# Kernel tuning notes

Hardware: AMD Instinct MI355X
Metric: run time of the kernel (lower is better)

## Reference

```python
import jax, jax.numpy as jnp
import numpy as np

B, N, D_IN, H, D_OUT = 64, 512, 1024, 1024, 1024
EPS = 1e-5          # torch BatchNorm1d default eps
NEG_SLOPE = 0.01    # torch leaky_relu default


def setup_inputs() -> dict:
    key = jax.random.key(0)
    ks = jax.random.split(key, 12)
    s_in = 1.0 / np.sqrt(D_IN)
    s_h = 1.0 / np.sqrt(H)
    return {
        "x": jax.random.normal(ks[0], (B, N, D_IN), dtype=jnp.float32),
        # weights stored as [in, out] so y = x @ W + b
        "W1": jax.random.uniform(ks[1], (D_IN, H), jnp.float32, -s_in, s_in),
        "b1": jax.random.uniform(ks[2], (H,), jnp.float32, -s_in, s_in),
        "gamma": jnp.ones((N,), jnp.float32),
        "beta": jnp.zeros((N,), jnp.float32),
        "W2": jax.random.uniform(ks[3], (D_IN, H), jnp.float32, -s_in, s_in),
        "b2": jax.random.uniform(ks[4], (H,), jnp.float32, -s_in, s_in),
        "W3": jax.random.uniform(ks[5], (H, D_OUT), jnp.float32, -s_h, s_h),
        "b3": jax.random.uniform(ks[6], (D_OUT,), jnp.float32, -s_h, s_h),
        "W4": jax.random.uniform(ks[7], (D_IN, D_OUT), jnp.float32, -s_in, s_in),
        "b4": jax.random.uniform(ks[8], (D_OUT,), jnp.float32, -s_in, s_in),
    }


def reference(x, W1, b1, gamma, beta, W2, b2, W3, b3, W4, b4):
    h = W1.shape[1]
    # theta_x = leaky_relu(bn(l1(x)))
    t = x @ W1 + b1                                   # [B, N, H]
    # BatchNorm1d(num_input): channel dim is N; train-mode batch stats over (B, H)
    mean = jnp.mean(t, axis=(0, 2), keepdims=True)
    var = jnp.var(t, axis=(0, 2), keepdims=True)      # biased variance (torch norm path)
    t = gamma[None, :, None] * (t - mean) * jax.lax.rsqrt(var + EPS) + beta[None, :, None]
    t = jnp.where(t >= 0, t, NEG_SLOPE * t)
    # sigma = theta @ M @ theta^T with M = (I - 1/h)/h  ==  mean-center rows then scale by 1/h
    tM = (t - jnp.mean(t, axis=-1, keepdims=True)) / h  # [B, N, H]
    sigma = jnp.einsum("bnh,bmh->bnm", tM, t)           # [B, N, N]
    att = sigma / jnp.sqrt(jnp.float32(h))              # normal_factor = sqrt(hidden)
    # GLOBAL softmax over the full flattened N*N matrix per batch element
    bsz, n = x.shape[0], x.shape[1]
    att = jax.nn.softmax(att.reshape(bsz, -1), axis=1).reshape(bsz, n, n)
    g = x @ W2 + b2                                     # [B, N, H]
    p = jnp.einsum("bnm,bmh->bnh", att, g) @ W3 + b3    # [B, N, D_OUT]
    phi = x @ W4 + b4                                   # [B, N, D_OUT]
    return phi + p
```

## Files before the change

kernel.cpp:

```cpp
#include <hip/hip_runtime.h>
#include <hip/hip_bf16.h>

typedef _Float16 f16x8 __attribute__((ext_vector_type(8)));
typedef _Float16 f16x4 __attribute__((ext_vector_type(4)));
typedef float    f32x4 __attribute__((ext_vector_type(4)));

#define EPS_ 1e-5f

__device__ __forceinline__ void gload_lds16(const _Float16* g, _Float16* l) {
    __builtin_amdgcn_global_load_lds(
        (const __attribute__((address_space(1))) void*)g,
        (__attribute__((address_space(3))) void*)l, 16, 0, 0);
}


__global__ void k_cvt_f16(const float* __restrict__ in, _Float16* __restrict__ out, int n4) {
    int i = blockIdx.x * blockDim.x + threadIdx.x;
    int stride = gridDim.x * blockDim.x;
    const float4* in4 = (const float4*)in;
    for (; i < n4; i += stride) {
        float4 v = in4[i];
        f16x4 o;
        o[0] = (_Float16)v.x; o[1] = (_Float16)v.y;
        o[2] = (_Float16)v.z; o[3] = (_Float16)v.w;
        *(f16x4*)(out + (size_t)i * 4) = o;
    }
}

__global__ void k_transpose_w(const float* __restrict__ in, _Float16* __restrict__ out) {
    __shared__ float tile[32][33];
    int bx = blockIdx.x * 32;
    int by = blockIdx.y * 32;
    int tx = threadIdx.x, ty = threadIdx.y;
    #pragma unroll
    for (int r = 0; r < 32; r += 8)
        tile[ty + r][tx] = in[(size_t)(by + ty + r) * 1024 + bx + tx];
    __syncthreads();
    #pragma unroll
    for (int r = 0; r < 32; r += 8)
        out[(size_t)(bx + ty + r) * 1024 + by + tx] = (_Float16)tile[tx][ty + r];
}

__global__ void k_b23(const float* __restrict__ b2, const float* __restrict__ W3,
                      float* __restrict__ b23) {
    const int oo = threadIdx.x & 63, hc = threadIdx.x >> 6;
    const int o = blockIdx.x * 64 + oo;
    float s = 0.f;
    for (int h = hc * 256; h < hc * 256 + 256; ++h) s += b2[h] * W3[(size_t)h * 1024 + o];
    __shared__ float red[4][64];
    red[hc][oo] = s;
    __syncthreads();
    if (threadIdx.x < 64) {
        int o2 = blockIdx.x * 64 + threadIdx.x;
        b23[o2] = red[0][threadIdx.x] + red[1][threadIdx.x] + red[2][threadIdx.x] + red[3][threadIdx.x];
    }
}


__global__ void k_bnstats(const _Float16* __restrict__ t, const float* __restrict__ gamma,
                          const float* __restrict__ beta, float* __restrict__ scale,
                          float* __restrict__ shift) {
    const int n = blockIdx.x, tid = threadIdx.x;
    float s = 0.f, s2 = 0.f;
    const _Float16* base = t + (size_t)n * 1024 + tid * 4;
    for (int b = 0; b < 64; ++b) {
        f16x4 v = *(const f16x4*)(base + (size_t)b * 512 * 1024);
        float x0 = (float)v[0], x1 = (float)v[1], x2 = (float)v[2], x3 = (float)v[3];
        s  += x0 + x1 + x2 + x3;
        s2 += x0 * x0 + x1 * x1 + x2 * x2 + x3 * x3;
    }
    #pragma unroll
    for (int o = 32; o > 0; o >>= 1) { s += __shfl_down(s, o); s2 += __shfl_down(s2, o); }
    __shared__ float rs_[4], rs2_[4];
    int lane = tid & 63, w = tid >> 6;
    if (lane == 0) { rs_[w] = s; rs2_[w] = s2; }
    __syncthreads();
    if (tid == 0) {
        float S  = rs_[0] + rs_[1] + rs_[2] + rs_[3];
        float S2 = rs2_[0] + rs2_[1] + rs2_[2] + rs2_[3];
        float mean = S * (1.f / 65536.f);
        float var  = S2 * (1.f / 65536.f) - mean * mean;
        float r = rsqrtf(var + EPS_);
        float sc = gamma[n] * r;
        scale[n] = sc;
        shift[n] = beta[n] - mean * sc;
    }
}

__global__ void k_bnorm(const _Float16* __restrict__ t, const float* __restrict__ scale,
                        const float* __restrict__ shift, _Float16* __restrict__ theta,
                        float* __restrict__ mu) {
    const int row = blockIdx.x, tid = threadIdx.x;
    const int n = row & 511;
    const float sc = scale[n], sh = shift[n];
    f16x4 v = *(const f16x4*)(t + (size_t)row * 1024 + tid * 4);
    float a0 = fmaf((float)v[0], sc, sh); a0 = a0 >= 0.f ? a0 : 0.01f * a0;
    float a1 = fmaf((float)v[1], sc, sh); a1 = a1 >= 0.f ? a1 : 0.01f * a1;
    float a2 = fmaf((float)v[2], sc, sh); a2 = a2 >= 0.f ? a2 : 0.01f * a2;
    float a3 = fmaf((float)v[3], sc, sh); a3 = a3 >= 0.f ? a3 : 0.01f * a3;
    float s = a0 + a1 + a2 + a3;
    #pragma unroll
    for (int o = 32; o > 0; o >>= 1) s += __shfl_down(s, o);
    __shared__ float red[4];
    int lane = tid & 63, w = tid >> 6;
    if (lane == 0) red[w] = s;
    __syncthreads();
    const float mean = (red[0] + red[1] + red[2] + red[3]) * (1.f / 1024.f);
    f16x4 th;
    th[0] = (_Float16)a0; th[1] = (_Float16)a1; th[2] = (_Float16)a2; th[3] = (_Float16)a3;
    *(f16x4*)(theta + (size_t)row * 1024 + tid * 4) = th;
    if (tid == 0) mu[row] = mean;
}

__global__ void k_ssum(const float* __restrict__ part, float* __restrict__ rsum,
                       float* __restrict__ ssum) {
    const int b = blockIdx.x, j = threadIdx.x;
    const int idx = b * 512 + j;
    float s = part[idx] + part[32768 + idx] + part[65536 + idx] + part[98304 + idx];
    rsum[idx] = s;
    #pragma unroll
    for (int o = 32; o > 0; o >>= 1) s += __shfl_down(s, o);
    __shared__ float red[8];
    if ((j & 63) == 0) red[j >> 6] = s;
    __syncthreads();
    if (j == 0) {
        float tt = 0.f;
        #pragma unroll
        for (int k = 0; k < 8; k++) tt += red[k];
        ssum[b] = tt;
    }
}


template <int MODE>
__global__ __launch_bounds__(256) void k_gemm(
    const _Float16* __restrict__ A0, const _Float16* __restrict__ B0,
    const float* __restrict__ auxA, float* __restrict__ auxW,
    void* __restrict__ outp) {

    constexpr int BK = 32;
    __shared__ _Float16 Al[4096];
    __shared__ _Float16 Bl[4096];

    const int tid = threadIdx.x, lane = tid & 63, w = tid >> 6;
    const int wm = w >> 1, wn = w & 1;
    const int bm = blockIdx.x, bn = blockIdx.y, bz = blockIdx.z;

    const int srow = tid >> 2;
    const int skofs = ((tid & 3) ^ ((tid >> 3) & 3)) * 8;
    _Float16* lA0 = &Al[(w * 64) * 8];
    _Float16* lA1 = &Al[(256 + w * 64) * 8];
    _Float16* lB0 = &Bl[(w * 64) * 8];
    _Float16* lB1 = &Bl[(256 + w * 64) * 8];

    const int lr = lane & 15, kg = lane >> 4;
    const int kswz = kg ^ ((lr >> 1) & 3);

    f32x4 acc[4][4] = {};

    const size_t aO = ((size_t)bz * 512 + bm * 128) * 1024;
    const size_t bO = ((size_t)bz * 512 + bn * 128) * 1024;
    for (int k0 = 0; k0 < 1024; k0 += BK) {
        gload_lds16(A0 + aO + (size_t)srow * 1024 + k0 + skofs, lA0);
        gload_lds16(A0 + aO + (size_t)(srow + 64) * 1024 + k0 + skofs, lA1);
        gload_lds16(B0 + bO + (size_t)srow * 1024 + k0 + skofs, lB0);
        gload_lds16(B0 + bO + (size_t)(srow + 64) * 1024 + k0 + skofs, lB1);
        __syncthreads();
        f16x8 af[4], bf[4];
        #pragma unroll
        for (int m = 0; m < 4; m++)
            af[m] = *(const f16x8*)&Al[((wm * 64 + m * 16 + lr) * 4 + kswz) * 8];
        #pragma unroll
        for (int n = 0; n < 4; n++)
            bf[n] = *(const f16x8*)&Bl[((wn * 64 + n * 16 + lr) * 4 + kswz) * 8];
        #pragma unroll
        for (int m = 0; m < 4; m++)
            #pragma unroll
            for (int n = 0; n < 4; n++)
                acc[m][n] = __builtin_amdgcn_mfma_f32_16x16x32_f16(af[m], bf[n], acc[m][n], 0, 0, 0);
        __syncthreads();
    }

    if constexpr (MODE == 1) {
        __shared__ float rbuf[2][128];
        _Float16* o = (_Float16*)outp + (size_t)bz * 262144;
        #pragma unroll
        for (int m = 0; m < 4; m++) {
            const int r0 = wm * 64 + m * 16 + kg * 4;
            float rs[4] = {0.f, 0.f, 0.f, 0.f};
            #pragma unroll
            for (int n = 0; n < 4; n++) {
                const int gc = bn * 128 + wn * 64 + n * 16 + lr;
                const float mj = auxA[bz * 512 + gc];
                #pragma unroll
                for (int i = 0; i < 4; i++) {
                    const float mi = auxA[bz * 512 + bm * 128 + r0 + i];
                    const float e = __expf(acc[m][n][i] * (1.f / 32768.f) - mi * mj * (1.f / 32.f));
                    o[(size_t)(bm * 128 + r0 + i) * 512 + gc] = (_Float16)e;
                    rs[i] += e;
                }
            }
            #pragma unroll
            for (int i = 0; i < 4; i++) {
                float v = rs[i];
                v += __shfl_xor(v, 1); v += __shfl_xor(v, 2);
                v += __shfl_xor(v, 4); v += __shfl_xor(v, 8);
                if (lr == 0) rbuf[wn][r0 + i] = v;
            }
        }
        __syncthreads();
        if (tid < 128)
            auxW[(size_t)bn * 32768 + bz * 512 + bm * 128 + tid] = rbuf[0][tid] + rbuf[1][tid];
    } else {
        _Float16* o = (_Float16*)outp;
        #pragma unroll
        for (int m = 0; m < 4; m++) {
            #pragma unroll
            for (int n = 0; n < 4; n++) {
                const int r0 = wm * 64 + m * 16 + kg * 4;
                const int gc = bn * 128 + wn * 64 + n * 16 + lr;
                #pragma unroll
                for (int i = 0; i < 4; i++)
                    o[(size_t)(bm * 128 + r0 + i) * 1024 + gc] = (_Float16)acc[m][n][i];
            }
        }
    }
}


template <int MODE>
__global__ __launch_bounds__(512) void k_gemm8(
    const _Float16* __restrict__ A0, const _Float16* __restrict__ B0,
    const _Float16* __restrict__ A1, const _Float16* __restrict__ B1,
    const float* __restrict__ biasf, const float* __restrict__ biasg,
    const float* __restrict__ auxA, const float* __restrict__ auxB,
    const float* __restrict__ sumptr, void* __restrict__ outp) {

    __shared__ _Float16 LA[32768];
    __shared__ _Float16 LB[32768];

    const int tid = threadIdx.x, lane = tid & 63, wid = tid >> 6;
    const int wm = wid >> 2, wn = wid & 3;
    const int lr = lane & 15, kq = lane >> 4;

    const int swz = (blockIdx.x & 7) * 64 + (blockIdx.x >> 3);
    int bm, bn, bz = 0;
    if constexpr (MODE == 3) { bz = swz >> 3; bm = (swz >> 2) & 1; bn = swz & 3; }
    else { bm = swz >> 2; bn = swz & 3; }

    constexpr int NITER = (MODE == 3) ? 12 : 8;
    float oscale = 1.f;
    if constexpr (MODE == 3) oscale = 1.f / sumptr[bz];

    const int i0 = tid >> 3;
    const int kgs = (tid & 7) ^ (i0 & 7);

    auto STAGE = [&](int g, int isA, int h) {
        const _Float16* P; int ld; size_t off; int kk;
        if constexpr (MODE == 3) {
            if (g < 8) {
                kk = g * 64;
                if (isA) { P = A0; ld = 512;  off = (size_t)bz * 262144 + (size_t)bm * 256 * 512; }
                else     { P = B0; ld = 512;  off = (size_t)bz * 524288 + (size_t)bn * 256 * 512; }
            } else {
                kk = (g - 8) * 64;
                if (isA) { P = A1; ld = 1024; off = ((size_t)bz * 512 + bm * 256) * 1024; }
                else     { P = B1; ld = 1024; off = (size_t)bn * 256 * 1024; }
            }
        } else {
            kk = g * 64;
            if (isA) { P = A0; ld = 1024; off = (size_t)bm * 256 * 1024; }
            else     { P = B0; ld = 1024; off = (size_t)bn * 256 * 1024; }
        }
        const int l0 = isA ? (h * 64 + i0)
                           : ((i0 >> 5) * 64 + h * 32 + (i0 & 31));
        const int l1 = isA ? (128 + h * 64 + i0)
                           : (((i0 >> 5) + 2) * 64 + h * 32 + (i0 & 31));
        _Float16* dst = (isA ? LA : LB) + ((g & 1) * 2 + h) * 8192 + wid * 512;
        gload_lds16(P + off + (size_t)l0 * ld + kk + kgs * 8, dst);
        gload_lds16(P + off + (size_t)l1 * ld + kk + kgs * 8, dst + 4096);
    };

    f32x4 acc[8][4] = {};

    STAGE(0, 1, 0); STAGE(0, 0, 0); STAGE(0, 0, 1); STAGE(0, 1, 1);
    STAGE(1, 0, 0); STAGE(1, 0, 1); STAGE(1, 1, 0);
    asm volatile("s_waitcnt vmcnt(6)" ::: "memory");
    __builtin_amdgcn_s_barrier();

    for (int i = 0; i < NITER; ++i) {
        if constexpr (MODE == 3) {
            if (i == 4) {
                #pragma unroll
                for (int m = 0; m < 8; m++)
                    #pragma unroll
                    for (int n = 0; n < 4; n++)
                        #pragma unroll
                        for (int v = 0; v < 4; v++) acc[m][n][v] *= oscale;
            }
        }
        const bool more = (i + 1 < NITER);
        #pragma unroll
        for (int kt = 0; kt < 2; ++kt) {
            f16x8 bf[4][2];
            #pragma unroll
            for (int sub = 0; sub < 4; ++sub) {
                const int ph = kt * 4 + sub;
                if (sub == 0) {
                    #pragma unroll
                    for (int n = 0; n < 4; n++) {
                        const _Float16* Bs = LB + (kt * 2 + (n >> 1)) * 8192;
                        #pragma unroll
                        for (int s = 0; s < 2; s++)
                            bf[n][s] = *(const f16x8*)&Bs[(wn * 32 + (n & 1) * 16 + lr) * 64
                                                           + ((((s << 2) | kq) ^ (lr & 7)) << 3)];
                    }
                }
                const _Float16* As = LA + (kt * 2 + (sub >> 1)) * 8192;
                f16x8 af[2][2];
                #pragma unroll
                for (int j = 0; j < 2; j++) {
                    const int m = sub * 2 + j;
                    #pragma unroll
                    for (int s = 0; s < 2; s++)
                        af[j][s] = *(const f16x8*)&As[(wm * 64 + (m & 3) * 16 + lr) * 64
                                                       + ((((s << 2) | kq) ^ (lr & 7)) << 3)];
                }
                {
                    constexpr int gof[8] = {1, 2, 2, 2, 2, 3, 3, 3};
                    constexpr int isa[8] = {1, 0, 0, 1, 1, 0, 0, 1};
                    constexpr int hh [8] = {1, 0, 1, 0, 1, 0, 1, 0};
                    if (ph == 0 || more) STAGE(2 * i + gof[ph], isa[ph], hh[ph]);
                }
                __builtin_amdgcn_s_barrier();
                asm volatile("s_waitcnt lgkmcnt(0)" ::: "memory");
                __builtin_amdgcn_sched_barrier(0);
                __builtin_amdgcn_s_setprio(1);
                #pragma unroll
                for (int j = 0; j < 2; j++)
                    #pragma unroll
                    for (int n = 0; n < 4; n++)
                        #pragma unroll
                        for (int s = 0; s < 2; s++)
                            acc[sub * 2 + j][n] = __builtin_amdgcn_mfma_f32_16x16x32_f16(
                                af[j][s], bf[n][s], acc[sub * 2 + j][n], 0, 0, 0);
                __builtin_amdgcn_s_setprio(0);
                if (ph == 1) { if (more) asm volatile("s_waitcnt vmcnt(10)" ::: "memory");
                               else      asm volatile("s_waitcnt vmcnt(8)"  ::: "memory"); }
                if (ph == 3) { if (more) asm volatile("s_waitcnt vmcnt(8)"  ::: "memory");
                               else      asm volatile("s_waitcnt vmcnt(2)"  ::: "memory"); }
                if (ph == 5) { if (more) asm volatile("s_waitcnt vmcnt(10)" ::: "memory");
                               else      asm volatile("s_waitcnt vmcnt(0)"  ::: "memory"); }
                if (ph == 7) { if (more) asm volatile("s_waitcnt vmcnt(8)"  ::: "memory"); }
                __builtin_amdgcn_s_barrier();
            }
        }
    }

    #pragma unroll
    for (int m = 0; m < 8; m++) {
        #pragma unroll
        for (int n = 0; n < 4; n++) {
            const int gc = bn * 256 + wn * 64 + n * 16 + lr;
            const int gr0 = bm * 256 + wm * 128 + m * 16 + kq * 4;
            if constexpr (MODE == 0) {
                _Float16* o = (_Float16*)outp;
                const float bias = biasf[gc];
                #pragma unroll
                for (int i = 0; i < 4; i++)
                    o[(size_t)(gr0 + i) * 1024 + gc] = (_Float16)(acc[m][n][i] + bias);
            } else if constexpr (MODE == 2) {
                _Float16* o = (_Float16*)outp;
                const int bb = gr0 >> 9, mm = gr0 & 511;
                f16x4 pk;
                #pragma unroll
                for (int i = 0; i < 4; i++) pk[i] = (_Float16)acc[m][n][i];
                *(f16x4*)(o + ((size_t)bb * 1024 + gc) * 512 + mm) = pk;
            } else {
                float* o = (float*)outp;
                const float tail = biasf[gc] + biasg[gc];
                const float b23v = auxB[gc];
                #pragma unroll
                for (int i = 0; i < 4; i++) {
                    const int row = gr0 + i;
                    o[((size_t)bz * 512 + row) * 1024 + gc] =
                        acc[m][n][i] + auxA[bz * 512 + row] * oscale * b23v + tail;
                }
            }
        }
    }
}


extern "C" void kernel_launch(void* const* d_in, const int* in_sizes, int n_in,
                              void* d_out, int out_size, void* d_ws, size_t ws_size,
                              hipStream_t stream) {
    (void)in_sizes; (void)n_in; (void)out_size; (void)ws_size;
    const float* x     = (const float*)d_in[0];
    const float* W1    = (const float*)d_in[1];
    const float* b1    = (const float*)d_in[2];
    const float* gamma = (const float*)d_in[3];
    const float* beta  = (const float*)d_in[4];
    const float* W2    = (const float*)d_in[5];
    const float* b2    = (const float*)d_in[6];
    const float* W3    = (const float*)d_in[7];
    const float* b3    = (const float*)d_in[8];
    const float* W4    = (const float*)d_in[9];
    const float* b4    = (const float*)d_in[10];

    char* wsb = (char*)d_ws;
    const size_t MB = 1024 * 1024;
    _Float16* xb    = (_Float16*)(wsb);
    _Float16* W1t   = (_Float16*)(wsb + 64 * MB);
    _Float16* W3t   = (_Float16*)(wsb + 66 * MB);
    _Float16* W4t   = (_Float16*)(wsb + 68 * MB);
    _Float16* W2h   = (_Float16*)(wsb + 70 * MB);
    _Float16* W23t  = (_Float16*)(wsb + 72 * MB);
    float*    b23   = (float*)(wsb + 74 * MB);
    float*    scl   = (float*)(wsb + 74 * MB + 8192);
    float*    shf   = (float*)(wsb + 74 * MB + 16384);
    float*    ssum  = (float*)(wsb + 74 * MB + 24576);
    float*    mu    = (float*)(wsb + 75 * MB);
    float*    rsum  = (float*)(wsb + 76 * MB);
    float*    rpart = (float*)(wsb + 77 * MB);
    _Float16* t     = (_Float16*)(wsb + 80 * MB);
    _Float16* theta = (_Float16*)(wsb + 144 * MB);
    _Float16* att   = (_Float16*)(wsb + 208 * MB);
    _Float16* gwt   = (_Float16*)(wsb + 240 * MB);

    k_cvt_f16<<<8192, 256, 0, stream>>>(x, xb, 64 * 512 * 1024 / 4);
    k_cvt_f16<<<1024, 256, 0, stream>>>(W2, W2h, 1024 * 1024 / 4);
    dim3 tb(32, 8), tg(32, 32);
    k_transpose_w<<<tg, tb, 0, stream>>>(W1, W1t);
    k_transpose_w<<<tg, tb, 0, stream>>>(W3, W3t);
    k_transpose_w<<<tg, tb, 0, stream>>>(W4, W4t);
    k_gemm<5><<<dim3(8, 8, 1), 256, 0, stream>>>(W3t, W2h, nullptr, nullptr, W23t);
    k_b23<<<16, 256, 0, stream>>>(b2, W3, b23);
    k_gemm8<0><<<512, 512, 0, stream>>>(xb, W1t, nullptr, nullptr,
        b1, nullptr, nullptr, nullptr, nullptr, t);
    k_bnstats<<<512, 256, 0, stream>>>(t, gamma, beta, scl, shf);
    k_bnorm<<<32768, 256, 0, stream>>>(t, scl, shf, theta, mu);
    k_gemm<1><<<dim3(4, 4, 64), 256, 0, stream>>>(theta, theta, mu, rpart, att);
    k_ssum<<<64, 512, 0, stream>>>(rpart, rsum, ssum);
    k_gemm8<2><<<512, 512, 0, stream>>>(xb, W23t, nullptr, nullptr,
        nullptr, nullptr, nullptr, nullptr, nullptr, gwt);
    k_gemm8<3><<<512, 512, 0, stream>>>(att, gwt, xb, W4t,
        b3, b4, rsum, b23, ssum, d_out);
}
```

Baseline: 463.2 us.

## Exploit sigma symmetry in attention GEMM and software-pipeline LDS reads in gemm8

The attention GEMM now launches only upper-triangular 128x128 tiles per batch (10 of 16) and mirrors off-diagonal results into the transposed position, also writing column sums as row partial sums for the mirrored tile. This cuts MFMA work for the symmetric theta·theta^T product by about 40%, at the cost of strided transposed fp16 stores. Separately, the big gemm8 kernel is restructured to prefetch the next phase's A/B fragments from LDS right after issuing the current MFMAs, with the barrier and vmcnt waits moved. The point is to overlap LDS reads with matrix math.

```diff
diff --git a/kernel.cpp b/kernel.cpp
--- a/kernel.cpp
+++ b/kernel.cpp
@@ -144,7 +144,18 @@
 
     const int tid = threadIdx.x, lane = tid & 63, w = tid >> 6;
     const int wm = w >> 1, wn = w & 1;
-    const int bm = blockIdx.x, bn = blockIdx.y, bz = blockIdx.z;
+
+    int bm, bn, bz;
+    if constexpr (MODE == 1) {
+        const int p = blockIdx.x;
+        if (p < 4)      { bm = 0; bn = p; }
+        else if (p < 7) { bm = 1; bn = p - 3; }
+        else if (p < 9) { bm = 2; bn = p - 5; }
+        else            { bm = 3; bn = 3; }
+        bz = blockIdx.z;
+    } else {
+        bm = blockIdx.x; bn = blockIdx.y; bz = blockIdx.z;
+    }
 
     const int srow = tid >> 2;
     const int skofs = ((tid & 3) ^ ((tid >> 3) & 3)) * 8;
@@ -183,7 +194,10 @@
 
     if constexpr (MODE == 1) {
         __shared__ float rbuf[2][128];
+        __shared__ float cbuf[2][128];
+        const bool diag = (bm == bn);
         _Float16* o = (_Float16*)outp + (size_t)bz * 262144;
+        float csn[4] = {0.f, 0.f, 0.f, 0.f};
         #pragma unroll
         for (int m = 0; m < 4; m++) {
             const int r0 = wm * 64 + m * 16 + kg * 4;
@@ -197,7 +211,10 @@
                     const float mi = auxA[bz * 512 + bm * 128 + r0 + i];
                     const float e = __expf(acc[m][n][i] * (1.f / 32768.f) - mi * mj * (1.f / 32.f));
                     o[(size_t)(bm * 128 + r0 + i) * 512 + gc] = (_Float16)e;
+                    if (!diag)
+                        o[(size_t)gc * 512 + bm * 128 + r0 + i] = (_Float16)e;
                     rs[i] += e;
+                    csn[n] += e;
                 }
             }
             #pragma unroll
@@ -208,9 +225,20 @@
                 if (lr == 0) rbuf[wn][r0 + i] = v;
             }
         }
+        if (!diag) {
+            #pragma unroll
+            for (int n = 0; n < 4; n++) {
+                float v = csn[n];
+                v += __shfl_xor(v, 16); v += __shfl_xor(v, 32);
+                if (kg == 0) cbuf[wm][wn * 64 + n * 16 + lr] = v;
+            }
+        }
         __syncthreads();
-        if (tid < 128)
+        if (tid < 128) {
             auxW[(size_t)bn * 32768 + bz * 512 + bm * 128 + tid] = rbuf[0][tid] + rbuf[1][tid];
+            if (!diag)
+                auxW[(size_t)bm * 32768 + bz * 512 + bn * 128 + tid] = cbuf[0][tid] + cbuf[1][tid];
+        }
     } else {
         _Float16* o = (_Float16*)outp;
         #pragma unroll
@@ -281,12 +309,39 @@
         gload_lds16(P + off + (size_t)l1 * ld + kk + kgs * 8, dst + 4096);
     };
 
+    f16x8 bf[4][2];
+    f16x8 af[2][2];
+
+    auto RD_B = [&](int ktp) {
+        #pragma unroll
+        for (int n = 0; n < 4; n++) {
+            const _Float16* Bs = LB + (ktp * 2 + (n >> 1)) * 8192;
+            #pragma unroll
+            for (int s = 0; s < 2; s++)
+                bf[n][s] = *(const f16x8*)&Bs[(wn * 32 + (n & 1) * 16 + lr) * 64
+                                               + ((((s << 2) | kq) ^ (lr & 7)) << 3)];
+        }
+    };
+    auto RD_A = [&](int ktp, int sub) {
+        const _Float16* As = LA + (ktp * 2 + (sub >> 1)) * 8192;
+        #pragma unroll
+        for (int j = 0; j < 2; j++) {
+            const int m = sub * 2 + j;
+            #pragma unroll
+            for (int s = 0; s < 2; s++)
+                af[j][s] = *(const f16x8*)&As[(wm * 64 + (m & 3) * 16 + lr) * 64
+                                               + ((((s << 2) | kq) ^ (lr & 7)) << 3)];
+        }
+    };
+
     f32x4 acc[8][4] = {};
 
-    STAGE(0, 1, 0); STAGE(0, 0, 0); STAGE(0, 0, 1); STAGE(0, 1, 1);
+    STAGE(0, 0, 0); STAGE(0, 0, 1); STAGE(0, 1, 0);
+    STAGE(0, 1, 1);
     STAGE(1, 0, 0); STAGE(1, 0, 1); STAGE(1, 1, 0);
-    asm volatile("s_waitcnt vmcnt(6)" ::: "memory");
+    asm volatile("s_waitcnt vmcnt(8)" ::: "memory");
     __builtin_amdgcn_s_barrier();
+    RD_B(0); RD_A(0, 0);
 
     for (int i = 0; i < NITER; ++i) {
         if constexpr (MODE == 3) {
@@ -301,58 +356,38 @@
         }
         const bool more = (i + 1 < NITER);
         #pragma unroll
-        for (int kt = 0; kt < 2; ++kt) {
-            f16x8 bf[4][2];
-            #pragma unroll
-            for (int sub = 0; sub < 4; ++sub) {
-                const int ph = kt * 4 + sub;
-                if (sub == 0) {
-                    #pragma unroll
-                    for (int n = 0; n < 4; n++) {
-                        const _Float16* Bs = LB + (kt * 2 + (n >> 1)) * 8192;
-                        #pragma unroll
-                        for (int s = 0; s < 2; s++)
-                            bf[n][s] = *(const f16x8*)&Bs[(wn * 32 + (n & 1) * 16 + lr) * 64
-                                                           + ((((s << 2) | kq) ^ (lr & 7)) << 3)];
-                    }
-                }
-                const _Float16* As = LA + (kt * 2 + (sub >> 1)) * 8192;
-                f16x8 af[2][2];
-                #pragma unroll
-                for (int j = 0; j < 2; j++) {
-                    const int m = sub * 2 + j;
+        for (int ph = 0; ph < 8; ++ph) {
+            const int sub = ph & 3;
+            __builtin_amdgcn_s_barrier();
+            asm volatile("s_waitcnt lgkmcnt(0)" ::: "memory");
+            __builtin_amdgcn_sched_barrier(0);
+            __builtin_amdgcn_s_setprio(1);
+            #pragma unroll
+            for (int j = 0; j < 2; j++)
+                #pragma unroll
+                for (int n = 0; n < 4; n++)
                     #pragma unroll
                     for (int s = 0; s < 2; s++)
-                        af[j][s] = *(const f16x8*)&As[(wm * 64 + (m & 3) * 16 + lr) * 64
-                                                       + ((((s << 2) | kq) ^ (lr & 7)) << 3)];
-                }
-                {
-                    constexpr int gof[8] = {1, 2, 2, 2, 2, 3, 3, 3};
-                    constexpr int isa[8] = {1, 0, 0, 1, 1, 0, 0, 1};
-                    constexpr int hh [8] = {1, 0, 1, 0, 1, 0, 1, 0};
-                    if (ph == 0 || more) STAGE(2 * i + gof[ph], isa[ph], hh[ph]);
-                }
-                __builtin_amdgcn_s_barrier();
-                asm volatile("s_waitcnt lgkmcnt(0)" ::: "memory");
-                __builtin_amdgcn_sched_barrier(0);
-                __builtin_amdgcn_s_setprio(1);
-                #pragma unroll
-                for (int j = 0; j < 2; j++)
-                    #pragma unroll
-                    for (int n = 0; n < 4; n++)
-                        #pragma unroll
-                        for (int s = 0; s < 2; s++)
-                            acc[sub * 2 + j][n] = __builtin_amdgcn_mfma_f32_16x16x32_f16(
-                                af[j][s], bf[n][s], acc[sub * 2 + j][n], 0, 0, 0);
-                __builtin_amdgcn_s_setprio(0);
-                if (ph == 1) { if (more) asm volatile("s_waitcnt vmcnt(10)" ::: "memory");
-                               else      asm volatile("s_waitcnt vmcnt(8)"  ::: "memory"); }
-                if (ph == 3) { if (more) asm volatile("s_waitcnt vmcnt(8)"  ::: "memory");
-                               else      asm volatile("s_waitcnt vmcnt(2)"  ::: "memory"); }
-                if (ph == 5) { if (more) asm volatile("s_waitcnt vmcnt(10)" ::: "memory");
-                               else      asm volatile("s_waitcnt vmcnt(0)"  ::: "memory"); }
-                if (ph == 7) { if (more) asm volatile("s_waitcnt vmcnt(8)"  ::: "memory"); }
-                __builtin_amdgcn_s_barrier();
+                        acc[sub * 2 + j][n] = __builtin_amdgcn_mfma_f32_16x16x32_f16(
+                            af[j][s], bf[n][s], acc[sub * 2 + j][n], 0, 0, 0);
+            __builtin_amdgcn_s_setprio(0);
+            if (ph == 1) asm volatile("s_waitcnt vmcnt(8)" ::: "memory");
+            if (ph == 3) { if (more) asm volatile("s_waitcnt vmcnt(6)" ::: "memory");
+                           else      asm volatile("s_waitcnt vmcnt(2)" ::: "memory"); }
+            if (ph == 5) { if (more) asm volatile("s_waitcnt vmcnt(8)" ::: "memory");
+                           else      asm volatile("s_waitcnt vmcnt(0)" ::: "memory"); }
+            if (ph == 7 && more) asm volatile("s_waitcnt vmcnt(6)" ::: "memory");
+            if (ph < 7) {
+                if (ph == 3) RD_B(1);
+                RD_A((ph + 1) >> 2, (ph + 1) & 3);
+            } else if (more) {
+                RD_B(0); RD_A(0, 0);
+            }
+            {
+                constexpr int gof[8] = {1, 2, 2, 2, 2, 3, 3, 3};
+                constexpr int isa[8] = {1, 0, 0, 1, 1, 0, 0, 1};
+                constexpr int hh [8] = {1, 0, 1, 0, 1, 0, 1, 0};
+                if (more || ph == 0) STAGE(2 * i + gof[ph], isa[ph], hh[ph]);
             }
         }
     }
@@ -440,7 +475,7 @@
         b1, nullptr, nullptr, nullptr, nullptr, t);
     k_bnstats<<<512, 256, 0, stream>>>(t, gamma, beta, scl, shf);
     k_bnorm<<<32768, 256, 0, stream>>>(t, scl, shf, theta, mu);
-    k_gemm<1><<<dim3(4, 4, 64), 256, 0, stream>>>(theta, theta, mu, rpart, att);
+    k_gemm<1><<<dim3(10, 1, 64), 256, 0, stream>>>(theta, theta, mu, rpart, att);
     k_ssum<<<64, 512, 0, stream>>>(rpart, rsum, ssum);
     k_gemm8<2><<<512, 512, 0, stream>>>(xb, W23t, nullptr, nullptr,
         nullptr, nullptr, nullptr, nullptr, nullptr, gwt);
```

Result: no change. 470.2 us (+1.5%).

## Fuse W1 and W23 GEMMs into one launch and exploit symmetric sigma

Applied to the files above, without the earlier changes.

Concatenates W1t and W23t into one weight buffer so a single GEMM over x produces both t (with bias) and the transposed g output, removing one launch and one extra pass over x. The sigma/att GEMM now computes only the upper-triangular 128x128 tiles (10 of 16 per batch). Each off-diagonal tile writes its transpose through an LDS staging buffer and also writes column sums into the row-sum partials. This relies on the exp term being symmetric, which holds because sigma is theta·theta^T with a symmetric mean correction. It adds LDS use and an extra transposed store in exchange for about 37% fewer MFMA tiles.

```diff
diff --git a/kernel.cpp b/kernel.cpp
--- a/kernel.cpp
+++ b/kernel.cpp
@@ -144,7 +144,18 @@
 
     const int tid = threadIdx.x, lane = tid & 63, w = tid >> 6;
     const int wm = w >> 1, wn = w & 1;
-    const int bm = blockIdx.x, bn = blockIdx.y, bz = blockIdx.z;
+
+    int bm, bn, bz;
+    if constexpr (MODE == 1) {
+        const int p = blockIdx.x;
+        if (p < 4)      { bm = 0; bn = p; }
+        else if (p < 7) { bm = 1; bn = p - 3; }
+        else if (p < 9) { bm = 2; bn = p - 5; }
+        else            { bm = 3; bn = 3; }
+        bz = blockIdx.z;
+    } else {
+        bm = blockIdx.x; bn = blockIdx.y; bz = blockIdx.z;
+    }
 
     const int srow = tid >> 2;
     const int skofs = ((tid & 3) ^ ((tid >> 3) & 3)) * 8;
@@ -183,22 +194,31 @@
 
     if constexpr (MODE == 1) {
         __shared__ float rbuf[2][128];
+        __shared__ float cbuf[2][128];
+        __shared__ _Float16 T[128][136];
+        const bool diag = (bm == bn);
         _Float16* o = (_Float16*)outp + (size_t)bz * 262144;
+        float csn[4] = {0.f, 0.f, 0.f, 0.f};
         #pragma unroll
         for (int m = 0; m < 4; m++) {
             const int r0 = wm * 64 + m * 16 + kg * 4;
             float rs[4] = {0.f, 0.f, 0.f, 0.f};
             #pragma unroll
             for (int n = 0; n < 4; n++) {
-                const int gc = bn * 128 + wn * 64 + n * 16 + lr;
+                const int cl = wn * 64 + n * 16 + lr;
+                const int gc = bn * 128 + cl;
                 const float mj = auxA[bz * 512 + gc];
+                f16x4 pk;
                 #pragma unroll
                 for (int i = 0; i < 4; i++) {
                     const float mi = auxA[bz * 512 + bm * 128 + r0 + i];
                     const float e = __expf(acc[m][n][i] * (1.f / 32768.f) - mi * mj * (1.f / 32.f));
                     o[(size_t)(bm * 128 + r0 + i) * 512 + gc] = (_Float16)e;
+                    pk[i] = (_Float16)e;
                     rs[i] += e;
-                }
+                    csn[n] += e;
+                }
+                if (!diag) *(f16x4*)&T[cl][r0] = pk;
             }
             #pragma unroll
             for (int i = 0; i < 4; i++) {
@@ -208,9 +228,29 @@
                 if (lr == 0) rbuf[wn][r0 + i] = v;
             }
         }
+        if (!diag) {
+            #pragma unroll
+            for (int n = 0; n < 4; n++) {
+                float v = csn[n];
+                v += __shfl_xor(v, 16); v += __shfl_xor(v, 32);
+                if (kg == 0) cbuf[wm][wn * 64 + n * 16 + lr] = v;
+            }
+        }
         __syncthreads();
-        if (tid < 128)
+        if (tid < 128) {
             auxW[(size_t)bn * 32768 + bz * 512 + bm * 128 + tid] = rbuf[0][tid] + rbuf[1][tid];
+            if (!diag)
+                auxW[(size_t)bm * 32768 + bz * 512 + bn * 128 + tid] = cbuf[0][tid] + cbuf[1][tid];
+        }
+        if (!diag) {
+            #pragma unroll
+            for (int k = 0; k < 8; k++) {
+                const int q = k * 256 + tid;
+                const int c = q >> 4, j = q & 15;
+                f16x8 v = *(const f16x8*)&T[c][j * 8];
+                *(f16x8*)(o + (size_t)(bn * 128 + c) * 512 + bm * 128 + j * 8) = v;
+            }
+        }
     } else {
         _Float16* o = (_Float16*)outp;
         #pragma unroll
@@ -243,10 +283,15 @@
     const int wm = wid >> 2, wn = wid & 3;
     const int lr = lane & 15, kq = lane >> 4;
 
-    const int swz = (blockIdx.x & 7) * 64 + (blockIdx.x >> 3);
     int bm, bn, bz = 0;
-    if constexpr (MODE == 3) { bz = swz >> 3; bm = (swz >> 2) & 1; bn = swz & 3; }
-    else { bm = swz >> 2; bn = swz & 3; }
+    if constexpr (MODE == 6) {
+        const int swz = (blockIdx.x & 7) * 128 + (blockIdx.x >> 3);
+        bm = swz >> 3; bn = swz & 7;
+    } else {
+        const int swz = (blockIdx.x & 7) * 64 + (blockIdx.x >> 3);
+        if constexpr (MODE == 3) { bz = swz >> 3; bm = (swz >> 2) & 1; bn = swz & 3; }
+        else { bm = swz >> 2; bn = swz & 3; }
+    }
 
     constexpr int NITER = (MODE == 3) ? 12 : 8;
     float oscale = 1.f;
@@ -363,19 +408,22 @@
         for (int n = 0; n < 4; n++) {
             const int gc = bn * 256 + wn * 64 + n * 16 + lr;
             const int gr0 = bm * 256 + wm * 128 + m * 16 + kq * 4;
-            if constexpr (MODE == 0) {
-                _Float16* o = (_Float16*)outp;
-                const float bias = biasf[gc];
-                #pragma unroll
-                for (int i = 0; i < 4; i++)
-                    o[(size_t)(gr0 + i) * 1024 + gc] = (_Float16)(acc[m][n][i] + bias);
-            } else if constexpr (MODE == 2) {
-                _Float16* o = (_Float16*)outp;
-                const int bb = gr0 >> 9, mm = gr0 & 511;
-                f16x4 pk;
-                #pragma unroll
-                for (int i = 0; i < 4; i++) pk[i] = (_Float16)acc[m][n][i];
-                *(f16x4*)(o + ((size_t)bb * 1024 + gc) * 512 + mm) = pk;
+            if constexpr (MODE == 6) {
+                if (gc < 1024) {
+                    _Float16* o = (_Float16*)outp;
+                    const float bias = biasf[gc];
+                    #pragma unroll
+                    for (int i = 0; i < 4; i++)
+                        o[(size_t)(gr0 + i) * 1024 + gc] = (_Float16)(acc[m][n][i] + bias);
+                } else {
+                    _Float16* o = (_Float16*)B1;
+                    const int oc = gc - 1024;
+                    const int bb = gr0 >> 9, mm = gr0 & 511;
+                    f16x4 pk;
+                    #pragma unroll
+                    for (int i = 0; i < 4; i++) pk[i] = (_Float16)acc[m][n][i];
+                    *(f16x4*)(o + ((size_t)bb * 1024 + oc) * 512 + mm) = pk;
+                }
             } else {
                 float* o = (float*)outp;
                 const float tail = biasf[gc] + biasg[gc];
@@ -411,11 +459,12 @@
     char* wsb = (char*)d_ws;
     const size_t MB = 1024 * 1024;
     _Float16* xb    = (_Float16*)(wsb);
-    _Float16* W1t   = (_Float16*)(wsb + 64 * MB);
-    _Float16* W3t   = (_Float16*)(wsb + 66 * MB);
-    _Float16* W4t   = (_Float16*)(wsb + 68 * MB);
-    _Float16* W2h   = (_Float16*)(wsb + 70 * MB);
-    _Float16* W23t  = (_Float16*)(wsb + 72 * MB);
+    _Float16* Wcat  = (_Float16*)(wsb + 64 * MB);
+    _Float16* W1t   = Wcat;
+    _Float16* W23t  = Wcat + 1024 * 1024;
+    _Float16* W3t   = (_Float16*)(wsb + 68 * MB);
+    _Float16* W4t   = (_Float16*)(wsb + 70 * MB);
+    _Float16* W2h   = (_Float16*)(wsb + 72 * MB);
     float*    b23   = (float*)(wsb + 74 * MB);
     float*    scl   = (float*)(wsb + 74 * MB + 8192);
     float*    shf   = (float*)(wsb + 74 * MB + 16384);
@@ -436,14 +485,12 @@
     k_transpose_w<<<tg, tb, 0, stream>>>(W4, W4t);
     k_gemm<5><<<dim3(8, 8, 1), 256, 0, stream>>>(W3t, W2h, nullptr, nullptr, W23t);
     k_b23<<<16, 256, 0, stream>>>(b2, W3, b23);
-    k_gemm8<0><<<512, 512, 0, stream>>>(xb, W1t, nullptr, nullptr,
+    k_gemm8<6><<<1024, 512, 0, stream>>>(xb, Wcat, nullptr, gwt,
         b1, nullptr, nullptr, nullptr, nullptr, t);
     k_bnstats<<<512, 256, 0, stream>>>(t, gamma, beta, scl, shf);
     k_bnorm<<<32768, 256, 0, stream>>>(t, scl, shf, theta, mu);
-    k_gemm<1><<<dim3(4, 4, 64), 256, 0, stream>>>(theta, theta, mu, rpart, att);
+    k_gemm<1><<<dim3(10, 1, 64), 256, 0, stream>>>(theta, theta, mu, rpart, att);
     k_ssum<<<64, 512, 0, stream>>>(rpart, rsum, ssum);
-    k_gemm8<2><<<512, 512, 0, stream>>>(xb, W23t, nullptr, nullptr,
-        nullptr, nullptr, nullptr, nullptr, nullptr, gwt);
     k_gemm8<3><<<512, 512, 0, stream>>>(att, gwt, xb, W4t,
         b3, b4, rsum, b23, ssum, d_out);
 }
```

Result: faster. 449.2 us (-3.0%).
